# Optimization experiments

Hardware: AMD Instinct MI355X
Metric: run time of the kernel (lower is better)

## Reference

```python
import jax, jax.numpy as jnp
import numpy as np

N_NODES = 50000
N_EDGES = 800000
NODE_FEAT = 3
HID = 64
L = 4


def setup_inputs() -> dict:
    key = jax.random.key(0)
    ks = jax.random.split(key, 16)
    s = 0.05  # init scale
    inp = {
        'node_pos': jax.random.normal(ks[0], (N_NODES, 3), jnp.float32),
        'node_features': jax.random.normal(ks[1], (N_NODES, NODE_FEAT), jnp.float32),
        'edge_index': jax.random.randint(ks[2], (2, N_EDGES), 0, N_NODES, jnp.int64),
        # encoders
        'enc_w': jax.random.normal(ks[3], (NODE_FEAT, HID), jnp.float32) * s,
        'enc_b': jnp.zeros((HID,), jnp.float32),
        'edge_enc_w': jax.random.normal(ks[4], (3, HID), jnp.float32) * s,
        'edge_enc_b': jnp.zeros((HID,), jnp.float32),
        # stacked per-layer GNOLayer params
        'ew1': jax.random.normal(ks[5], (L, 3 * HID, HID), jnp.float32) * s,
        'eb1': jnp.zeros((L, HID), jnp.float32),
        'ew2': jax.random.normal(ks[6], (L, HID, HID), jnp.float32) * s,
        'eb2': jnp.zeros((L, HID), jnp.float32),
        'nw1': jax.random.normal(ks[7], (L, 2 * HID, HID), jnp.float32) * s,
        'nb1': jnp.zeros((L, HID), jnp.float32),
        'nw2': jax.random.normal(ks[8], (L, HID, HID), jnp.float32) * s,
        'nb2': jnp.zeros((L, HID), jnp.float32),
        # decoder
        'dec_w': jax.random.normal(ks[9], (HID, 1), jnp.float32) * s,
        'dec_b': jnp.zeros((1,), jnp.float32),
    }
    return inp


def reference(node_pos, node_features, edge_index, enc_w, enc_b, edge_enc_w,
              edge_enc_b, ew1, eb1, ew2, eb2, nw1, nb1, nw2, nb2, dec_w, dec_b):
    src, dst = edge_index[0], edge_index[1]
    edge_vec = node_pos[dst] - node_pos[src]            # [E, 3]
    h = node_features @ enc_w + enc_b                   # [N, H]
    e = edge_vec @ edge_enc_w + edge_enc_b              # [E, H]

    def layer(h, p):
        w1, b1, w2, b2, m1, c1, m2, c2 = p
        edge_in = jnp.concatenate([h[src], h[dst], e], axis=-1)   # [E, 3H]
        msg = jax.nn.relu(edge_in @ w1 + b1) @ w2 + b2            # [E, H]
        agg = jax.ops.segment_sum(msg, dst, num_segments=N_NODES)  # [N, H]
        node_in = jnp.concatenate([h, agg], axis=-1)              # [N, 2H]
        return jax.nn.relu(node_in @ m1 + c1) @ m2 + c2, None

    h, _ = jax.lax.scan(layer, h, (ew1, eb1, ew2, eb2, nw1, nb1, nw2, nb2))
    return h @ dec_w + dec_b                            # [N, 1]
```

## Files before the change

### kernel.cpp

```cpp
#include <hip/hip_runtime.h>

#define N_NODES 50000
#define N_EDGES 800000
#define HID 64
#define LAYERS 4
#define EP_NPB 32
#define EP_CAP 2048

typedef unsigned short u16;
typedef __attribute__((ext_vector_type(8))) __bf16 bf16x8;
typedef __attribute__((ext_vector_type(8))) unsigned short u16x8;
typedef __attribute__((ext_vector_type(4))) float f32x4;
typedef _Float16 h2 __attribute__((ext_vector_type(2)));

__device__ __forceinline__ u16 f2bf(float f) {
  unsigned u = __builtin_bit_cast(unsigned, f);
  u += 0x7fffu + ((u >> 16) & 1u);
  return (u16)(u >> 16);
}
__device__ __forceinline__ float bf2f(u16 s) {
  return __builtin_bit_cast(float, ((unsigned)s) << 16);
}
__device__ __forceinline__ u16 f2h(float f) {
  return __builtin_bit_cast(u16, (_Float16)f);
}
__device__ __forceinline__ unsigned pkadd(unsigned a, unsigned b) {
  h2 r = __builtin_bit_cast(h2, a) + __builtin_bit_cast(h2, b);
  return __builtin_bit_cast(unsigned, r);
}
__device__ __forceinline__ unsigned pkmax0(unsigned x) {
  unsigned r, z = 0u;
  asm("v_pk_max_f16 %0, %1, %2" : "=v"(r) : "v"(x), "v"(z));
  return r;
}

__global__ __launch_bounds__(256) void init_kernel(
    const float* __restrict__ nf, const float* __restrict__ enc_w,
    const float* __restrict__ enc_b,
    const float* __restrict__ ew1, const float* __restrict__ eb1,
    const float* __restrict__ ew2, const float* __restrict__ eb2,
    const float* __restrict__ nw1, const float* __restrict__ nw2,
    const float* __restrict__ edge_enc_w, const float* __restrict__ edge_enc_b,
    u16* __restrict__ h, u16* W1abT, float* Wvx, float* b1x,
    u16* NB1T, float* bb2, u16* M2T, int* __restrict__ cnt) {
  const int T = gridDim.x * 256;
  int tid = blockIdx.x * 256 + threadIdx.x;
  for (int i = tid; i < N_NODES; i += T) cnt[i] = 0;
  {
    const int szA = LAYERS * 128 * 64, szV = LAYERS * 3 * 64, szB = LAYERS * 64;
    const int szN = LAYERS * 64 * 128, szb2 = LAYERS * 64, szM = LAYERS * 64 * 64;
    const int tot = szA + szV + szB + szN + szb2 + szM;
    for (int i = tid; i < tot; i += T) {
      int idx = i;
      if (idx < szA) {
        int l = idx / (128 * 64); int r = idx % (128 * 64);
        int nfc = r / 64; int k = r % 64;
        int half = nfc >> 6, f = nfc & 63;
        W1abT[idx] = f2bf(ew1[(l * 192 + half * 64 + k) * 64 + f]);
        continue;
      }
      idx -= szA;
      if (idx < szV) {
        int l = idx / 192, r = idx % 192, a = r / 64, f = r % 64;
        float s = 0.f;
        for (int m = 0; m < 64; ++m) s += edge_enc_w[a * 64 + m] * ew1[(l * 192 + 128 + m) * 64 + f];
        Wvx[idx] = s;
        continue;
      }
      idx -= szV;
      if (idx < szB) {
        int l = idx / 64, f = idx % 64;
        float s = eb1[l * 64 + f];
        for (int m = 0; m < 64; ++m) s += edge_enc_b[m] * ew1[(l * 192 + 128 + m) * 64 + f];
        b1x[idx] = s;
        continue;
      }
      idx -= szB;
      if (idx < szN) {
        int l = idx / 8192, r = idx % 8192, f = r / 128, k = r % 128;
        float v;
        if (k < 64) v = nw1[(l * 128 + k) * 64 + f];
        else {
          int j = k - 64; float s = 0.f;
          for (int g = 0; g < 64; ++g)
            s += ew2[(l * 64 + j) * 64 + g] * nw1[(l * 128 + 64 + g) * 64 + f];
          v = s;
        }
        NB1T[idx] = f2bf(v);
        continue;
      }
      idx -= szN;
      if (idx < szb2) {
        int l = idx / 64, f = idx % 64;
        float s = 0.f;
        for (int g = 0; g < 64; ++g) s += eb2[l * 64 + g] * nw1[(l * 128 + 64 + g) * 64 + f];
        bb2[idx] = s;
        continue;
      }
      idx -= szb2;
      int l = idx / 4096, r = idx % 4096, f = r / 64, k = r % 64;
      M2T[idx] = f2bf(nw2[(l * 64 + k) * 64 + f]);
    }
  }
  for (int i = tid; i < N_NODES * 8; i += T) {
    int n = i >> 3, j0 = (i & 7) * 8;
    float x0 = nf[n * 3 + 0], x1 = nf[n * 3 + 1], x2 = nf[n * 3 + 2];
    u16x8 v;
#pragma unroll
    for (int j = 0; j < 8; ++j) {
      int jj = j0 + j;
      float s = enc_b[jj] + x0 * enc_w[jj] + x1 * enc_w[64 + jj] + x2 * enc_w[128 + jj];
      v[j] = f2bf(s);
    }
    *(u16x8*)(h + (size_t)n * 64 + j0) = v;
  }
}

__global__ __launch_bounds__(256) void hist_kernel(const int* __restrict__ dstA,
                                                   int* __restrict__ cnt,
                                                   int* __restrict__ rank) {
  int idx = blockIdx.x * 256 + threadIdx.x;
  if (idx < N_EDGES) rank[idx] = atomicAdd(&cnt[dstA[idx]], 1);
}

#define SCAN_NBLK 25
__global__ __launch_bounds__(256) void scan1_kernel(const int* __restrict__ cnt,
                                                    int* __restrict__ offs,
                                                    int* __restrict__ partials) {
  __shared__ int sm[2048];
  __shared__ int ws2[256];
  int t = threadIdx.x, b = blockIdx.x;
  int base = b * 2048;
#pragma unroll
  for (int i = 0; i < 8; ++i) {
    int idx = base + i * 256 + t;
    sm[i * 256 + t] = (idx < N_NODES) ? cnt[idx] : 0;
  }
  __syncthreads();
  int loc[8]; int s = 0;
#pragma unroll
  for (int i = 0; i < 8; ++i) { loc[i] = s; s += sm[t * 8 + i]; }
  ws2[t] = s;
  __syncthreads();
  for (int off = 1; off < 256; off <<= 1) {
    int u = (t >= off) ? ws2[t - off] : 0;
    __syncthreads();
    ws2[t] += u;
    __syncthreads();
  }
  int tbase = (t > 0) ? ws2[t - 1] : 0;
  if (t == 255) partials[b] = ws2[255];
#pragma unroll
  for (int i = 0; i < 8; ++i) {
    int idx = base + t * 8 + i;
    if (idx < N_NODES) offs[idx] = tbase + loc[i];
  }
}

__global__ __launch_bounds__(256) void scan3_kernel(int* __restrict__ offs,
                                                    const int* __restrict__ partials) {
  __shared__ int pref;
  int blk = (blockIdx.x * 256) >> 11;
  if (threadIdx.x == 0) {
    int s = 0;
    for (int i = 0; i < blk; ++i) s += partials[i];
    pref = s;
  }
  __syncthreads();
  int idx = blockIdx.x * 256 + threadIdx.x;
  if (idx < N_NODES) offs[idx] += pref;
}

__global__ __launch_bounds__(256) void scatter_kernel(const int* __restrict__ ei,
                                                      const int* __restrict__ offs,
                                                      const int* __restrict__ rank,
                                                      int* __restrict__ srcB) {
  int idx = blockIdx.x * 256 + threadIdx.x;
  if (idx >= N_EDGES) return;
  int s = ei[idx], d = ei[N_EDGES + idx];
  srcB[offs[d] + rank[idx]] = s << 7;
}

__global__ __launch_bounds__(256) void su_kernel(const u16* __restrict__ h,
                                                 const u16* __restrict__ W1abT,
                                                 const float* __restrict__ Wvx,
                                                 const float* __restrict__ b1x,
                                                 const float* __restrict__ pos,
                                                 u16* __restrict__ Sarr,
                                                 u16* __restrict__ Uarr, int layer) {
  __shared__ float sPos[192];
  int t = threadIdx.x;
  int lane = t & 63, wvi = t >> 6;
  int n16 = lane & 15, quad = lane >> 4;
  int n0 = blockIdx.x * 64;
  if (t < 192) {
    int idx = n0 * 3 + t;
    sPos[t] = (idx < N_NODES * 3) ? pos[idx] : 0.f;
  }
  __syncthreads();

  bf16x8 B[2][2];
  float w0[2], w1[2], w2[2], bb[2]; bool isU[2];
#pragma unroll
  for (int nt = 0; nt < 2; ++nt) {
    int col = wvi * 32 + nt * 16 + n16;
    const u16* p = W1abT + (size_t)(layer * 128 + col) * 64 + quad * 8;
    B[nt][0] = __builtin_bit_cast(bf16x8, *(const u16x8*)(p));
    B[nt][1] = __builtin_bit_cast(bf16x8, *(const u16x8*)(p + 32));
    int f = col & 63; isU[nt] = col >= 64;
    w0[nt] = Wvx[(layer * 3 + 0) * 64 + f];
    w1[nt] = Wvx[(layer * 3 + 1) * 64 + f];
    w2[nt] = Wvx[(layer * 3 + 2) * 64 + f];
    bb[nt] = b1x[layer * 64 + f];
  }
  f32x4 acc[4][2];
#pragma unroll
  for (int m = 0; m < 4; ++m)
#pragma unroll
    for (int nt = 0; nt < 2; ++nt) acc[m][nt] = (f32x4){0.f, 0.f, 0.f, 0.f};

#pragma unroll
  for (int m = 0; m < 4; ++m) {
    int row = n0 + m * 16 + n16;
    if (row >= N_NODES) row = N_NODES - 1;
    const u16* hp = h + (size_t)row * 64 + quad * 8;
    bf16x8 a0 = __builtin_bit_cast(bf16x8, *(const u16x8*)(hp));
    bf16x8 a1 = __builtin_bit_cast(bf16x8, *(const u16x8*)(hp + 32));
#pragma unroll
    for (int nt = 0; nt < 2; ++nt) {
      acc[m][nt] = __builtin_amdgcn_mfma_f32_16x16x32_bf16(a0, B[nt][0], acc[m][nt], 0, 0, 0);
      acc[m][nt] = __builtin_amdgcn_mfma_f32_16x16x32_bf16(a1, B[nt][1], acc[m][nt], 0, 0, 0);
    }
  }
#pragma unroll
  for (int m = 0; m < 4; ++m)
#pragma unroll
    for (int nt = 0; nt < 2; ++nt) {
      int col = wvi * 32 + nt * 16 + n16;
      int f = col & 63;
#pragma unroll
      for (int r = 0; r < 4; ++r) {
        int e = m * 16 + quad * 4 + r;
        int grow = n0 + e;
        if (grow < N_NODES) {
          float P = sPos[e * 3] * w0[nt] + sPos[e * 3 + 1] * w1[nt] + sPos[e * 3 + 2] * w2[nt];
          if (!isU[nt]) Sarr[(size_t)grow * 64 + f] = f2h(acc[m][nt][r] - P);
          else          Uarr[(size_t)grow * 64 + f] = f2h(acc[m][nt][r] + P + bb[nt]);
        }
      }
    }
}

__global__ __launch_bounds__(256) void ep_kernel(const u16* __restrict__ Sarr,
                                                 const u16* __restrict__ Uarr,
                                                 const int* __restrict__ srcB,
                                                 const int* __restrict__ offs,
                                                 u16* __restrict__ aggH) {
  __shared__ int sIdx[EP_CAP];
  __shared__ int sOff[EP_NPB + 1];
  int t = threadIdx.x;
  int lane = t & 63, wvi = t >> 6;
  int c = lane & 31, half = lane >> 5;
  unsigned cbu = (unsigned)(c << 2);
  int d0b = blockIdx.x * EP_NPB;
  if (t <= EP_NPB) {
    int d = d0b + t;
    sOff[t] = (d < N_NODES) ? offs[d] : N_EDGES;
  }
  __syncthreads();
  int eS = sOff[0];
  int nE = sOff[EP_NPB] - eS;
  bool fit = (nE <= EP_CAP);
  if (fit) {
    for (int i = t; i < nE; i += 256) sIdx[i] = srcB[eS + i];
    if (t == 0 && nE < EP_CAP) sIdx[nE] = 0;
  }
  __syncthreads();

  const char* __restrict__ Sb = (const char*)Sarr;
  const char* __restrict__ Ub = (const char*)Uarr;
  for (int i = 0; i < 8; i += 2) {
    int lnA = wvi * 8 + i, lnB = lnA + 1;
    int dA = d0b + lnA, dB = d0b + lnB;
    int e0A = sOff[lnA], degA = sOff[lnA + 1] - e0A;
    int e0B = sOff[lnB], degB = sOff[lnB + 1] - e0B;
    int dAc = dA < N_NODES ? dA : N_NODES - 1;
    int dBc = dB < N_NODES ? dB : N_NODES - 1;
    unsigned upA = *(const unsigned*)(Ub + (size_t)dAc * 128 + cbu);
    unsigned upB = *(const unsigned*)(Ub + (size_t)dBc * 128 + cbu);
    float saA = 0.f, sbA = 0.f, saB = 0.f, sbB = 0.f;
    int relA = (degA > 0) ? (e0A - eS) : 0;
    int relB = (degB > 0) ? (e0B - eS) : 0;
    int g0A = (degA > 0) ? e0A : 0;
    int g0B = (degB > 0) ? e0B : 0;
    int degMin = degA < degB ? degA : degB;
    int degMax = degA > degB ? degA : degB;
    int fullr = degMin >> 4;
    int rmax = (degMax + 15) >> 4;
    if (fit) {
      int r = 0;
      for (; r < fullr; ++r) {
        int base = r * 16 + half;
        unsigned wA[8], wB[8];
#pragma unroll
        for (int k = 0; k < 8; ++k) {
          int j = base + 2 * k;
          unsigned oA = (unsigned)sIdx[relA + j] + cbu;
          wA[k] = *(const unsigned*)(Sb + oA);
          unsigned oB = (unsigned)sIdx[relB + j] + cbu;
          wB[k] = *(const unsigned*)(Sb + oB);
        }
        unsigned pA = 0u, pB = 0u;
#pragma unroll
        for (int k = 0; k < 8; ++k) {
          pA = pkadd(pA, pkmax0(pkadd(wA[k], upA)));
          pB = pkadd(pB, pkmax0(pkadd(wB[k], upB)));
        }
        h2 hA2 = __builtin_bit_cast(h2, pA);
        h2 hB2 = __builtin_bit_cast(h2, pB);
        saA += (float)hA2[0]; sbA += (float)hA2[1];
        saB += (float)hB2[0]; sbB += (float)hB2[1];
      }
      for (; r < rmax; ++r) {
        int base = r * 16 + half;
        unsigned wA[8], wB[8]; bool okA[8], okB[8];
#pragma unroll
        for (int k = 0; k < 8; ++k) {
          int j = base + 2 * k;
          okA[k] = j < degA;
          unsigned oA = (unsigned)sIdx[relA + (okA[k] ? j : 0)] + cbu;
          wA[k] = *(const unsigned*)(Sb + oA);
          okB[k] = j < degB;
          unsigned oB = (unsigned)sIdx[relB + (okB[k] ? j : 0)] + cbu;
          wB[k] = *(const unsigned*)(Sb + oB);
        }
        unsigned pA = 0u, pB = 0u;
#pragma unroll
        for (int k = 0; k < 8; ++k) {
          unsigned zA = pkmax0(pkadd(wA[k], upA));
          pA = pkadd(pA, okA[k] ? zA : 0u);
          unsigned zB = pkmax0(pkadd(wB[k], upB));
          pB = pkadd(pB, okB[k] ? zB : 0u);
        }
        h2 hA2 = __builtin_bit_cast(h2, pA);
        h2 hB2 = __builtin_bit_cast(h2, pB);
        saA += (float)hA2[0]; sbA += (float)hA2[1];
        saB += (float)hB2[0]; sbB += (float)hB2[1];
      }
    } else {
      for (int r = 0; r < rmax; ++r) {
        int base = r * 16 + half;
        unsigned wA[8], wB[8]; bool okA[8], okB[8];
#pragma unroll
        for (int k = 0; k < 8; ++k) {
          int j = base + 2 * k;
          okA[k] = j < degA;
          unsigned oA = (unsigned)srcB[g0A + (okA[k] ? j : 0)] + cbu;
          wA[k] = *(const unsigned*)(Sb + oA);
          okB[k] = j < degB;
          unsigned oB = (unsigned)srcB[g0B + (okB[k] ? j : 0)] + cbu;
          wB[k] = *(const unsigned*)(Sb + oB);
        }
        unsigned pA = 0u, pB = 0u;
#pragma unroll
        for (int k = 0; k < 8; ++k) {
          unsigned zA = pkmax0(pkadd(wA[k], upA));
          pA = pkadd(pA, okA[k] ? zA : 0u);
          unsigned zB = pkmax0(pkadd(wB[k], upB));
          pB = pkadd(pB, okB[k] ? zB : 0u);
        }
        h2 hA2 = __builtin_bit_cast(h2, pA);
        h2 hB2 = __builtin_bit_cast(h2, pB);
        saA += (float)hA2[0]; sbA += (float)hA2[1];
        saB += (float)hB2[0]; sbB += (float)hB2[1];
      }
    }
    saA += __shfl_xor(saA, 32);  sbA += __shfl_xor(sbA, 32);
    saB += __shfl_xor(saB, 32);  sbB += __shfl_xor(sbB, 32);
    if (half == 0) {
      if (dA < N_NODES) {
        unsigned pk = (unsigned)f2bf(saA) | ((unsigned)f2bf(sbA) << 16);
        *(unsigned*)((char*)aggH + (size_t)dA * 128 + cbu) = pk;
      }
      if (dB < N_NODES) {
        unsigned pk = (unsigned)f2bf(saB) | ((unsigned)f2bf(sbB) << 16);
        *(unsigned*)((char*)aggH + (size_t)dB * 128 + cbu) = pk;
      }
    }
  }
}

__global__ __launch_bounds__(256) void node_kernel(
    const u16* __restrict__ h, const u16* __restrict__ aggH,
    const int* __restrict__ cnt,
    const u16* __restrict__ NB1T, const float* __restrict__ nb1,
    const float* __restrict__ bb2,
    const u16* __restrict__ M2T, const float* __restrict__ nb2,
    u16* __restrict__ h2, int layer,
    const u16* __restrict__ W1abT, const float* __restrict__ Wvx,
    const float* __restrict__ b1x, const float* __restrict__ pos,
    u16* __restrict__ Sarr, u16* __restrict__ Uarr,
    const float* __restrict__ dec_w, const float* __restrict__ dec_b,
    float* __restrict__ out) {
  __shared__ u16 Hs[64 * 72];
  __shared__ float sDeg[64];
  __shared__ float sPos[192];
  __shared__ float sRed[64][4];
  int t = threadIdx.x;
  int lane = t & 63, wvi = t >> 6;
  int n16 = lane & 15, quad = lane >> 4;
  int F = wvi * 16;
  int n0 = blockIdx.x * 64;

  if (t < 64) {
    int gn = n0 + t;
    sDeg[t] = (gn < N_NODES) ? (float)cnt[gn] : 0.f;
  }
  if (t >= 64 && t < 256) {
    int i = t - 64;
    int idx = n0 * 3 + i;
    sPos[i] = (idx < N_NODES * 3) ? pos[idx] : 0.f;
  }

  bf16x8 B1[4], B2[2];
  {
    const u16* p = NB1T + (size_t)(layer * 64 + F + n16) * 128 + quad * 8;
#pragma unroll
    for (int ks = 0; ks < 4; ++ks) B1[ks] = __builtin_bit_cast(bf16x8, *(const u16x8*)(p + ks * 32));
    const u16* q = M2T + (size_t)(layer * 64 + F + n16) * 64 + quad * 8;
#pragma unroll
    for (int ks = 0; ks < 2; ++ks) B2[ks] = __builtin_bit_cast(bf16x8, *(const u16x8*)(q + ks * 32));
  }
  float bias1 = nb1[layer * 64 + F + n16];
  float bb2f = bb2[layer * 64 + F + n16];
  float bias2 = nb2[layer * 64 + F + n16];
  __syncthreads();

  f32x4 acc[4];
#pragma unroll
  for (int m = 0; m < 4; ++m) acc[m] = (f32x4){0.f, 0.f, 0.f, 0.f};
#pragma unroll
  for (int m = 0; m < 4; ++m) {
    int row = n0 + m * 16 + n16;
    if (row >= N_NODES) row = N_NODES - 1;
    const u16* hp = h + (size_t)row * 64 + quad * 8;
    const u16* ap = aggH + (size_t)row * 64 + quad * 8;
    bf16x8 a0 = __builtin_bit_cast(bf16x8, *(const u16x8*)(hp));
    bf16x8 a1 = __builtin_bit_cast(bf16x8, *(const u16x8*)(hp + 32));
    bf16x8 a2 = __builtin_bit_cast(bf16x8, *(const u16x8*)(ap));
    bf16x8 a3 = __builtin_bit_cast(bf16x8, *(const u16x8*)(ap + 32));
    acc[m] = __builtin_amdgcn_mfma_f32_16x16x32_bf16(a0, B1[0], acc[m], 0, 0, 0);
    acc[m] = __builtin_amdgcn_mfma_f32_16x16x32_bf16(a1, B1[1], acc[m], 0, 0, 0);
    acc[m] = __builtin_amdgcn_mfma_f32_16x16x32_bf16(a2, B1[2], acc[m], 0, 0, 0);
    acc[m] = __builtin_amdgcn_mfma_f32_16x16x32_bf16(a3, B1[3], acc[m], 0, 0, 0);
  }
#pragma unroll
  for (int m = 0; m < 4; ++m)
#pragma unroll
    for (int r = 0; r < 4; ++r) {
      int e = m * 16 + quad * 4 + r;
      float v = acc[m][r] + bias1 + sDeg[e] * bb2f;
      v = v > 0.f ? v : 0.f;
      Hs[e * 72 + F + n16] = f2bf(v);
    }
  __syncthreads();

  float c2[4][4];
#pragma unroll
  for (int m = 0; m < 4; ++m) {
    const u16* hp = Hs + (m * 16 + n16) * 72 + quad * 8;
    f32x4 c = (f32x4){0.f, 0.f, 0.f, 0.f};
#pragma unroll
    for (int ks = 0; ks < 2; ++ks) {
      bf16x8 a = __builtin_bit_cast(bf16x8, *(const u16x8*)(hp + ks * 32));
      c = __builtin_amdgcn_mfma_f32_16x16x32_bf16(a, B2[ks], c, 0, 0, 0);
    }
#pragma unroll
    for (int r = 0; r < 4; ++r) c2[m][r] = c[r] + bias2;
  }
  __syncthreads();

#pragma unroll
  for (int m = 0; m < 4; ++m)
#pragma unroll
    for (int r = 0; r < 4; ++r) {
      int e = m * 16 + quad * 4 + r;
      u16 hv = f2bf(c2[m][r]);
      Hs[e * 72 + F + n16] = hv;
      int gn = n0 + e;
      if (layer < LAYERS - 1 && gn < N_NODES)
        h2[(size_t)gn * 64 + F + n16] = hv;
    }
  __syncthreads();

  if (layer < LAYERS - 1) {
    int lp = layer + 1;
    bf16x8 B3[2][2];
    float w0[2], w1[2], w2[2], bb[2]; bool isU[2];
#pragma unroll
    for (int nt = 0; nt < 2; ++nt) {
      int col = wvi * 32 + nt * 16 + n16;
      const u16* p = W1abT + (size_t)(lp * 128 + col) * 64 + quad * 8;
      B3[nt][0] = __builtin_bit_cast(bf16x8, *(const u16x8*)(p));
      B3[nt][1] = __builtin_bit_cast(bf16x8, *(const u16x8*)(p + 32));
      int f = col & 63; isU[nt] = col >= 64;
      w0[nt] = Wvx[(lp * 3 + 0) * 64 + f];
      w1[nt] = Wvx[(lp * 3 + 1) * 64 + f];
      w2[nt] = Wvx[(lp * 3 + 2) * 64 + f];
      bb[nt] = b1x[lp * 64 + f];
    }
    f32x4 a3[4][2];
#pragma unroll
    for (int m = 0; m < 4; ++m)
#pragma unroll
      for (int nt = 0; nt < 2; ++nt) a3[m][nt] = (f32x4){0.f, 0.f, 0.f, 0.f};
#pragma unroll
    for (int m = 0; m < 4; ++m) {
      const u16* hp = Hs + (m * 16 + n16) * 72 + quad * 8;
      bf16x8 a0 = __builtin_bit_cast(bf16x8, *(const u16x8*)(hp));
      bf16x8 a1 = __builtin_bit_cast(bf16x8, *(const u16x8*)(hp + 32));
#pragma unroll
      for (int nt = 0; nt < 2; ++nt) {
        a3[m][nt] = __builtin_amdgcn_mfma_f32_16x16x32_bf16(a0, B3[nt][0], a3[m][nt], 0, 0, 0);
        a3[m][nt] = __builtin_amdgcn_mfma_f32_16x16x32_bf16(a1, B3[nt][1], a3[m][nt], 0, 0, 0);
      }
    }
#pragma unroll
    for (int m = 0; m < 4; ++m)
#pragma unroll
      for (int nt = 0; nt < 2; ++nt) {
        int col = wvi * 32 + nt * 16 + n16;
        int f = col & 63;
#pragma unroll
        for (int r = 0; r < 4; ++r) {
          int e = m * 16 + quad * 4 + r;
          int grow = n0 + e;
          if (grow < N_NODES) {
            float P = sPos[e * 3] * w0[nt] + sPos[e * 3 + 1] * w1[nt] + sPos[e * 3 + 2] * w2[nt];
            if (!isU[nt]) Sarr[(size_t)grow * 64 + f] = f2h(a3[m][nt][r] - P);
            else          Uarr[(size_t)grow * 64 + f] = f2h(a3[m][nt][r] + P + bb[nt]);
          }
        }
      }
  } else {
    int e = t >> 2, part = t & 3;
    float s = 0.f;
#pragma unroll
    for (int j = 0; j < 16; ++j)
      s += bf2f(Hs[e * 72 + part * 16 + j]) * dec_w[part * 16 + j];
    sRed[e][part] = s;
    __syncthreads();
    if (part == 0) {
      int gn = n0 + e;
      if (gn < N_NODES)
        out[gn] = sRed[e][0] + sRed[e][1] + sRed[e][2] + sRed[e][3] + dec_b[0];
    }
  }
}

extern "C" void kernel_launch(void* const* d_in, const int* in_sizes, int n_in,
                              void* d_out, int out_size, void* d_ws, size_t ws_size,
                              hipStream_t stream) {
  const float* node_pos   = (const float*)d_in[0];
  const float* node_feat  = (const float*)d_in[1];
  const int*   edge_index = (const int*)d_in[2];
  const float* enc_w      = (const float*)d_in[3];
  const float* enc_b      = (const float*)d_in[4];
  const float* edge_enc_w = (const float*)d_in[5];
  const float* edge_enc_b = (const float*)d_in[6];
  const float* ew1        = (const float*)d_in[7];
  const float* eb1        = (const float*)d_in[8];
  const float* ew2        = (const float*)d_in[9];
  const float* eb2        = (const float*)d_in[10];
  const float* nw1        = (const float*)d_in[11];
  const float* nb1        = (const float*)d_in[12];
  const float* nw2        = (const float*)d_in[13];
  const float* nb2        = (const float*)d_in[14];
  const float* dec_w      = (const float*)d_in[15];
  const float* dec_b      = (const float*)d_in[16];
  float* out = (float*)d_out;

  char* ws = (char*)d_ws;
  size_t off = 0;
  u16*    hA    = (u16*)(ws + off);    off += (size_t)N_NODES * 64 * 2;
  u16*    hB    = (u16*)(ws + off);    off += (size_t)N_NODES * 64 * 2;
  u16*    Sarr  = (u16*)(ws + off);    off += (size_t)N_NODES * 64 * 2;
  u16*    Uarr  = (u16*)(ws + off);    off += (size_t)N_NODES * 64 * 2;
  u16*    aggH  = (u16*)(ws + off);    off += (size_t)N_NODES * 64 * 2;
  u16*    W1abT = (u16*)(ws + off);    off += (size_t)LAYERS * 128 * 64 * 2;
  float*  Wvx   = (float*)(ws + off);  off += (size_t)LAYERS * 3 * 64 * 4;
  float*  b1x   = (float*)(ws + off);  off += (size_t)LAYERS * 64 * 4;
  u16*    NB1T  = (u16*)(ws + off);    off += (size_t)LAYERS * 64 * 128 * 2;
  float*  bb2   = (float*)(ws + off);  off += (size_t)LAYERS * 64 * 4;
  u16*    M2T   = (u16*)(ws + off);    off += (size_t)LAYERS * 64 * 64 * 2;
  int*    cnt      = (int*)(ws + off); off += (size_t)N_NODES * 4;
  int*    offsB    = (int*)(ws + off); off += (size_t)N_NODES * 4;
  int*    partials = (int*)(ws + off); off += 32 * 4;
  int*    rank     = (int*)(ws + off); off += (size_t)N_EDGES * 4;
  int*    srcB     = (int*)(ws + off); off += (size_t)N_EDGES * 4;

  const int* dstA = edge_index + N_EDGES;
  const int NBLK = (N_NODES + 63) / 64;
  const int EP_GRID = (N_NODES + EP_NPB - 1) / EP_NPB;

  init_kernel<<<1024, 256, 0, stream>>>(
      node_feat, enc_w, enc_b, ew1, eb1, ew2, eb2, nw1, nw2,
      edge_enc_w, edge_enc_b, hA, W1abT, Wvx, b1x, NB1T, bb2, M2T, cnt);

  hist_kernel<<<(N_EDGES + 255) / 256, 256, 0, stream>>>(dstA, cnt, rank);
  scan1_kernel<<<SCAN_NBLK, 256, 0, stream>>>(cnt, offsB, partials);
  scan3_kernel<<<(N_NODES + 255) / 256, 256, 0, stream>>>(offsB, partials);
  scatter_kernel<<<(N_EDGES + 255) / 256, 256, 0, stream>>>(edge_index, offsB, rank, srcB);

  su_kernel<<<NBLK, 256, 0, stream>>>(hA, W1abT, Wvx, b1x, node_pos, Sarr, Uarr, 0);

  u16* hcur = hA; u16* hnext = hB;
  for (int l = 0; l < LAYERS; ++l) {
    ep_kernel<<<EP_GRID, 256, 0, stream>>>(Sarr, Uarr, srcB, offsB, aggH);
    node_kernel<<<NBLK, 256, 0, stream>>>(hcur, aggH, cnt, NB1T, nb1, bb2, M2T, nb2,
                                          hnext, l, W1abT, Wvx, b1x, node_pos,
                                          Sarr, Uarr, dec_w, dec_b, out);
    u16* tmp = hcur; hcur = hnext; hnext = tmp;
  }
}
```

Before: 342.2 us.

## Fuse edge aggregation and node update into one per-layer kernel

Merges the per-layer edge-aggregation kernel and the node MLP kernel into one layer_kernel working on 32 nodes per block. The aggregate stays in shared memory instead of round-tripping through global memory. S/U buffers are now double-buffered so the fused kernel can read this layer's S/U while writing the next layer's. The node encoder also moves into the first S/U kernel, which uses a shared-memory tile of h. This saves a launch and a global write and read per layer, at the cost of a larger shared-memory footprint and half-size MFMA tiles in the node phase.

```diff
diff --git a/kernel.cpp b/kernel.cpp
--- a/kernel.cpp
+++ b/kernel.cpp
@@ -4,14 +4,14 @@
 #define N_EDGES 800000
 #define HID 64
 #define LAYERS 4
-#define EP_NPB 32
 #define EP_CAP 2048
+#define SCAN_NBLK 25
 
 typedef unsigned short u16;
 typedef __attribute__((ext_vector_type(8))) __bf16 bf16x8;
 typedef __attribute__((ext_vector_type(8))) unsigned short u16x8;
 typedef __attribute__((ext_vector_type(4))) float f32x4;
-typedef _Float16 h2 __attribute__((ext_vector_type(2)));
+typedef _Float16 f16x2 __attribute__((ext_vector_type(2)));
 
 __device__ __forceinline__ u16 f2bf(float f) {
   unsigned u = __builtin_bit_cast(unsigned, f);
@@ -25,7 +25,7 @@
   return __builtin_bit_cast(u16, (_Float16)f);
 }
 __device__ __forceinline__ unsigned pkadd(unsigned a, unsigned b) {
-  h2 r = __builtin_bit_cast(h2, a) + __builtin_bit_cast(h2, b);
+  f16x2 r = __builtin_bit_cast(f16x2, a) + __builtin_bit_cast(f16x2, b);
   return __builtin_bit_cast(unsigned, r);
 }
 __device__ __forceinline__ unsigned pkmax0(unsigned x) {
@@ -35,84 +35,68 @@
 }
 
 __global__ __launch_bounds__(256) void init_kernel(
-    const float* __restrict__ nf, const float* __restrict__ enc_w,
-    const float* __restrict__ enc_b,
     const float* __restrict__ ew1, const float* __restrict__ eb1,
     const float* __restrict__ ew2, const float* __restrict__ eb2,
     const float* __restrict__ nw1, const float* __restrict__ nw2,
     const float* __restrict__ edge_enc_w, const float* __restrict__ edge_enc_b,
-    u16* __restrict__ h, u16* W1abT, float* Wvx, float* b1x,
+    u16* W1abT, float* Wvx, float* b1x,
     u16* NB1T, float* bb2, u16* M2T, int* __restrict__ cnt) {
   const int T = gridDim.x * 256;
   int tid = blockIdx.x * 256 + threadIdx.x;
   for (int i = tid; i < N_NODES; i += T) cnt[i] = 0;
-  {
-    const int szA = LAYERS * 128 * 64, szV = LAYERS * 3 * 64, szB = LAYERS * 64;
-    const int szN = LAYERS * 64 * 128, szb2 = LAYERS * 64, szM = LAYERS * 64 * 64;
-    const int tot = szA + szV + szB + szN + szb2 + szM;
-    for (int i = tid; i < tot; i += T) {
-      int idx = i;
-      if (idx < szA) {
-        int l = idx / (128 * 64); int r = idx % (128 * 64);
-        int nfc = r / 64; int k = r % 64;
-        int half = nfc >> 6, f = nfc & 63;
-        W1abT[idx] = f2bf(ew1[(l * 192 + half * 64 + k) * 64 + f]);
-        continue;
+  const int szA = LAYERS * 128 * 64, szV = LAYERS * 3 * 64, szB = LAYERS * 64;
+  const int szN = LAYERS * 64 * 128, szb2 = LAYERS * 64, szM = LAYERS * 64 * 64;
+  const int tot = szA + szV + szB + szN + szb2 + szM;
+  for (int i = tid; i < tot; i += T) {
+    int idx = i;
+    if (idx < szA) {
+      int l = idx / (128 * 64); int r = idx % (128 * 64);
+      int nfc = r / 64; int k = r % 64;
+      int half = nfc >> 6, f = nfc & 63;
+      W1abT[idx] = f2bf(ew1[(l * 192 + half * 64 + k) * 64 + f]);
+      continue;
+    }
+    idx -= szA;
+    if (idx < szV) {
+      int l = idx / 192, r = idx % 192, a = r / 64, f = r % 64;
+      float s = 0.f;
+      for (int m = 0; m < 64; ++m) s += edge_enc_w[a * 64 + m] * ew1[(l * 192 + 128 + m) * 64 + f];
+      Wvx[idx] = s;
+      continue;
+    }
+    idx -= szV;
+    if (idx < szB) {
+      int l = idx / 64, f = idx % 64;
+      float s = eb1[l * 64 + f];
+      for (int m = 0; m < 64; ++m) s += edge_enc_b[m] * ew1[(l * 192 + 128 + m) * 64 + f];
+      b1x[idx] = s;
+      continue;
+    }
+    idx -= szB;
+    if (idx < szN) {
+      int l = idx / 8192, r = idx % 8192, f = r / 128, k = r % 128;
+      float v;
+      if (k < 64) v = nw1[(l * 128 + k) * 64 + f];
+      else {
+        int j = k - 64; float s = 0.f;
+        for (int g = 0; g < 64; ++g)
+          s += ew2[(l * 64 + j) * 64 + g] * nw1[(l * 128 + 64 + g) * 64 + f];
+        v = s;
       }
-      idx -= szA;
-      if (idx < szV) {
-        int l = idx / 192, r = idx % 192, a = r / 64, f = r % 64;
-        float s = 0.f;
-        for (int m = 0; m < 64; ++m) s += edge_enc_w[a * 64 + m] * ew1[(l * 192 + 128 + m) * 64 + f];
-        Wvx[idx] = s;
-        continue;
-      }
-      idx -= szV;
-      if (idx < szB) {
-        int l = idx / 64, f = idx % 64;
-        float s = eb1[l * 64 + f];
-        for (int m = 0; m < 64; ++m) s += edge_enc_b[m] * ew1[(l * 192 + 128 + m) * 64 + f];
-        b1x[idx] = s;
-        continue;
-      }
-      idx -= szB;
-      if (idx < szN) {
-        int l = idx / 8192, r = idx % 8192, f = r / 128, k = r % 128;
-        float v;
-        if (k < 64) v = nw1[(l * 128 + k) * 64 + f];
-        else {
-          int j = k - 64; float s = 0.f;
-          for (int g = 0; g < 64; ++g)
-            s += ew2[(l * 64 + j) * 64 + g] * nw1[(l * 128 + 64 + g) * 64 + f];
-          v = s;
-        }
-        NB1T[idx] = f2bf(v);
-        continue;
-      }
-      idx -= szN;
-      if (idx < szb2) {
-        int l = idx / 64, f = idx % 64;
-        float s = 0.f;
-        for (int g = 0; g < 64; ++g) s += eb2[l * 64 + g] * nw1[(l * 128 + 64 + g) * 64 + f];
-        bb2[idx] = s;
-        continue;
-      }
-      idx -= szb2;
-      int l = idx / 4096, r = idx % 4096, f = r / 64, k = r % 64;
-      M2T[idx] = f2bf(nw2[(l * 64 + k) * 64 + f]);
-    }
-  }
-  for (int i = tid; i < N_NODES * 8; i += T) {
-    int n = i >> 3, j0 = (i & 7) * 8;
-    float x0 = nf[n * 3 + 0], x1 = nf[n * 3 + 1], x2 = nf[n * 3 + 2];
-    u16x8 v;
-#pragma unroll
-    for (int j = 0; j < 8; ++j) {
-      int jj = j0 + j;
-      float s = enc_b[jj] + x0 * enc_w[jj] + x1 * enc_w[64 + jj] + x2 * enc_w[128 + jj];
-      v[j] = f2bf(s);
-    }
-    *(u16x8*)(h + (size_t)n * 64 + j0) = v;
+      NB1T[idx] = f2bf(v);
+      continue;
+    }
+    idx -= szN;
+    if (idx < szb2) {
+      int l = idx / 64, f = idx % 64;
+      float s = 0.f;
+      for (int g = 0; g < 64; ++g) s += eb2[l * 64 + g] * nw1[(l * 128 + 64 + g) * 64 + f];
+      bb2[idx] = s;
+      continue;
+    }
+    idx -= szb2;
+    int l = idx / 4096, r = idx % 4096, f = r / 64, k = r % 64;
+    M2T[idx] = f2bf(nw2[(l * 64 + k) * 64 + f]);
   }
 }
 
@@ -123,7 +107,6 @@
   if (idx < N_EDGES) rank[idx] = atomicAdd(&cnt[dstA[idx]], 1);
 }
 
-#define SCAN_NBLK 25
 __global__ __launch_bounds__(256) void scan1_kernel(const int* __restrict__ cnt,
                                                     int* __restrict__ offs,
                                                     int* __restrict__ partials) {
@@ -181,21 +164,44 @@
   srcB[offs[d] + rank[idx]] = s << 7;
 }
 
-__global__ __launch_bounds__(256) void su_kernel(const u16* __restrict__ h,
-                                                 const u16* __restrict__ W1abT,
-                                                 const float* __restrict__ Wvx,
-                                                 const float* __restrict__ b1x,
-                                                 const float* __restrict__ pos,
-                                                 u16* __restrict__ Sarr,
-                                                 u16* __restrict__ Uarr, int layer) {
+__global__ __launch_bounds__(256) void encsu_kernel(
+    const float* __restrict__ nf, const float* __restrict__ enc_w,
+    const float* __restrict__ enc_b,
+    const u16* __restrict__ W1abT, const float* __restrict__ Wvx,
+    const float* __restrict__ b1x, const float* __restrict__ pos,
+    u16* __restrict__ h, u16* __restrict__ Sarr, u16* __restrict__ Uarr) {
+  __shared__ u16 hT[64 * 72];
   __shared__ float sPos[192];
+  __shared__ float sNf[192];
   int t = threadIdx.x;
   int lane = t & 63, wvi = t >> 6;
   int n16 = lane & 15, quad = lane >> 4;
   int n0 = blockIdx.x * 64;
   if (t < 192) {
     int idx = n0 * 3 + t;
-    sPos[t] = (idx < N_NODES * 3) ? pos[idx] : 0.f;
+    bool ok = idx < N_NODES * 3;
+    sPos[t] = ok ? pos[idx] : 0.f;
+    sNf[t] = ok ? nf[idx] : 0.f;
+  }
+  __syncthreads();
+  {
+    int n = t >> 2, g = t & 3;
+    float x0 = sNf[n * 3], x1 = sNf[n * 3 + 1], x2 = sNf[n * 3 + 2];
+    u16x8 v0, v1;
+#pragma unroll
+    for (int j = 0; j < 8; ++j) {
+      int jj = g * 16 + j;
+      v0[j] = f2bf(enc_b[jj] + x0 * enc_w[jj] + x1 * enc_w[64 + jj] + x2 * enc_w[128 + jj]);
+      int jj2 = jj + 8;
+      v1[j] = f2bf(enc_b[jj2] + x0 * enc_w[jj2] + x1 * enc_w[64 + jj2] + x2 * enc_w[128 + jj2]);
+    }
+    *(u16x8*)(hT + n * 72 + g * 16) = v0;
+    *(u16x8*)(hT + n * 72 + g * 16 + 8) = v1;
+    int gn = n0 + n;
+    if (gn < N_NODES) {
+      *(u16x8*)(h + (size_t)gn * 64 + g * 16) = v0;
+      *(u16x8*)(h + (size_t)gn * 64 + g * 16 + 8) = v1;
+    }
   }
   __syncthreads();
 
@@ -204,26 +210,23 @@
 #pragma unroll
   for (int nt = 0; nt < 2; ++nt) {
     int col = wvi * 32 + nt * 16 + n16;
-    const u16* p = W1abT + (size_t)(layer * 128 + col) * 64 + quad * 8;
+    const u16* p = W1abT + (size_t)col * 64 + quad * 8;
     B[nt][0] = __builtin_bit_cast(bf16x8, *(const u16x8*)(p));
     B[nt][1] = __builtin_bit_cast(bf16x8, *(const u16x8*)(p + 32));
     int f = col & 63; isU[nt] = col >= 64;
-    w0[nt] = Wvx[(layer * 3 + 0) * 64 + f];
-    w1[nt] = Wvx[(layer * 3 + 1) * 64 + f];
-    w2[nt] = Wvx[(layer * 3 + 2) * 64 + f];
-    bb[nt] = b1x[layer * 64 + f];
+    w0[nt] = Wvx[f];
+    w1[nt] = Wvx[64 + f];
+    w2[nt] = Wvx[128 + f];
+    bb[nt] = b1x[f];
   }
   f32x4 acc[4][2];
 #pragma unroll
   for (int m = 0; m < 4; ++m)
 #pragma unroll
     for (int nt = 0; nt < 2; ++nt) acc[m][nt] = (f32x4){0.f, 0.f, 0.f, 0.f};
-
 #pragma unroll
   for (int m = 0; m < 4; ++m) {
-    int row = n0 + m * 16 + n16;
-    if (row >= N_NODES) row = N_NODES - 1;
-    const u16* hp = h + (size_t)row * 64 + quad * 8;
+    const u16* hp = hT + (m * 16 + n16) * 72 + quad * 8;
     bf16x8 a0 = __builtin_bit_cast(bf16x8, *(const u16x8*)(hp));
     bf16x8 a1 = __builtin_bit_cast(bf16x8, *(const u16x8*)(hp + 32));
 #pragma unroll
@@ -251,25 +254,43 @@
     }
 }
 
-__global__ __launch_bounds__(256) void ep_kernel(const u16* __restrict__ Sarr,
-                                                 const u16* __restrict__ Uarr,
-                                                 const int* __restrict__ srcB,
-                                                 const int* __restrict__ offs,
-                                                 u16* __restrict__ aggH) {
+__global__ __launch_bounds__(256) void layer_kernel(
+    const u16* __restrict__ h, const int* __restrict__ srcB,
+    const int* __restrict__ offs,
+    const u16* __restrict__ Sr, const u16* __restrict__ Ur,
+    const u16* __restrict__ NB1T, const float* __restrict__ nb1,
+    const float* __restrict__ bb2,
+    const u16* __restrict__ M2T, const float* __restrict__ nb2,
+    u16* __restrict__ hnext, int layer,
+    const u16* __restrict__ W1abT, const float* __restrict__ Wvx,
+    const float* __restrict__ b1x, const float* __restrict__ pos,
+    u16* __restrict__ Sw, u16* __restrict__ Uw,
+    const float* __restrict__ dec_w, const float* __restrict__ dec_b,
+    float* __restrict__ out) {
   __shared__ int sIdx[EP_CAP];
-  __shared__ int sOff[EP_NPB + 1];
+  __shared__ int sOff[33];
+  __shared__ u16 aggT[32 * 72];
+  __shared__ u16 Hs[32 * 72];
+  __shared__ float sPos[96];
+  __shared__ float sRed[32][8];
   int t = threadIdx.x;
   int lane = t & 63, wvi = t >> 6;
-  int c = lane & 31, half = lane >> 5;
-  unsigned cbu = (unsigned)(c << 2);
-  int d0b = blockIdx.x * EP_NPB;
-  if (t <= EP_NPB) {
-    int d = d0b + t;
+  int n16 = lane & 15, quad = lane >> 4;
+  int F = wvi * 16;
+  int n0 = blockIdx.x * 32;
+
+  if (t <= 32) {
+    int d = n0 + t;
     sOff[t] = (d < N_NODES) ? offs[d] : N_EDGES;
   }
+  if (t >= 64 && t < 160) {
+    int i = t - 64;
+    int idx = n0 * 3 + i;
+    sPos[i] = (idx < N_NODES * 3) ? pos[idx] : 0.f;
+  }
   __syncthreads();
   int eS = sOff[0];
-  int nE = sOff[EP_NPB] - eS;
+  int nE = sOff[32] - eS;
   bool fit = (nE <= EP_CAP);
   if (fit) {
     for (int i = t; i < nE; i += 256) sIdx[i] = srcB[eS + i];
@@ -277,150 +298,112 @@
   }
   __syncthreads();
 
-  const char* __restrict__ Sb = (const char*)Sarr;
-  const char* __restrict__ Ub = (const char*)Uarr;
-  for (int i = 0; i < 8; i += 2) {
-    int lnA = wvi * 8 + i, lnB = lnA + 1;
-    int dA = d0b + lnA, dB = d0b + lnB;
-    int e0A = sOff[lnA], degA = sOff[lnA + 1] - e0A;
-    int e0B = sOff[lnB], degB = sOff[lnB + 1] - e0B;
-    int dAc = dA < N_NODES ? dA : N_NODES - 1;
-    int dBc = dB < N_NODES ? dB : N_NODES - 1;
-    unsigned upA = *(const unsigned*)(Ub + (size_t)dAc * 128 + cbu);
-    unsigned upB = *(const unsigned*)(Ub + (size_t)dBc * 128 + cbu);
-    float saA = 0.f, sbA = 0.f, saB = 0.f, sbB = 0.f;
-    int relA = (degA > 0) ? (e0A - eS) : 0;
-    int relB = (degB > 0) ? (e0B - eS) : 0;
-    int g0A = (degA > 0) ? e0A : 0;
-    int g0B = (degB > 0) ? e0B : 0;
-    int degMin = degA < degB ? degA : degB;
-    int degMax = degA > degB ? degA : degB;
-    int fullr = degMin >> 4;
-    int rmax = (degMax + 15) >> 4;
-    if (fit) {
-      int r = 0;
-      for (; r < fullr; ++r) {
-        int base = r * 16 + half;
-        unsigned wA[8], wB[8];
-#pragma unroll
-        for (int k = 0; k < 8; ++k) {
-          int j = base + 2 * k;
-          unsigned oA = (unsigned)sIdx[relA + j] + cbu;
-          wA[k] = *(const unsigned*)(Sb + oA);
-          unsigned oB = (unsigned)sIdx[relB + j] + cbu;
-          wB[k] = *(const unsigned*)(Sb + oB);
+  {
+    int c = lane & 31, half = lane >> 5;
+    unsigned cbu = (unsigned)(c << 2);
+    const char* __restrict__ Sb = (const char*)Sr;
+    const char* __restrict__ Ub = (const char*)Ur;
+    for (int i = 0; i < 8; i += 2) {
+      int lnA = wvi * 8 + i;
+      int dA = n0 + lnA;
+      int e0A = sOff[lnA], degA = sOff[lnA + 1] - e0A;
+      int e0B = sOff[lnA + 1], degB = sOff[lnA + 2] - e0B;
+      int dAc = dA < N_NODES ? dA : N_NODES - 1;
+      int dBc = (dA + 1) < N_NODES ? (dA + 1) : N_NODES - 1;
+      unsigned upA = *(const unsigned*)(Ub + (size_t)dAc * 128 + cbu);
+      unsigned upB = *(const unsigned*)(Ub + (size_t)dBc * 128 + cbu);
+      float saA = 0.f, sbA = 0.f, saB = 0.f, sbB = 0.f;
+      int relA = (degA > 0) ? (e0A - eS) : 0;
+      int relB = (degB > 0) ? (e0B - eS) : 0;
+      int g0A = (degA > 0) ? e0A : 0;
+      int g0B = (degB > 0) ? e0B : 0;
+      int degMin = degA < degB ? degA : degB;
+      int degMax = degA > degB ? degA : degB;
+      int fullr = degMin >> 4;
+      int rmax = (degMax + 15) >> 4;
+      if (fit) {
+        int r = 0;
+        for (; r < fullr; ++r) {
+          int base = r * 16 + half;
+          unsigned wA[8], wB[8];
+#pragma unroll
+          for (int kk = 0; kk < 8; ++kk) {
+            int j = base + 2 * kk;
+            wA[kk] = *(const unsigned*)(Sb + (unsigned)sIdx[relA + j] + cbu);
+            wB[kk] = *(const unsigned*)(Sb + (unsigned)sIdx[relB + j] + cbu);
+          }
+          unsigned pA = 0u, pB = 0u;
+#pragma unroll
+          for (int kk = 0; kk < 8; ++kk) {
+            pA = pkadd(pA, pkmax0(pkadd(wA[kk], upA)));
+            pB = pkadd(pB, pkmax0(pkadd(wB[kk], upB)));
+          }
+          f16x2 hA2 = __builtin_bit_cast(f16x2, pA);
+          f16x2 hB2 = __builtin_bit_cast(f16x2, pB);
+          saA += (float)hA2[0]; sbA += (float)hA2[1];
+          saB += (float)hB2[0]; sbB += (float)hB2[1];
         }
-        unsigned pA = 0u, pB = 0u;
-#pragma unroll
-        for (int k = 0; k < 8; ++k) {
-          pA = pkadd(pA, pkmax0(pkadd(wA[k], upA)));
-          pB = pkadd(pB, pkmax0(pkadd(wB[k], upB)));
+        for (; r < rmax; ++r) {
+          int base = r * 16 + half;
+          unsigned wA[8], wB[8]; bool okA[8], okB[8];
+#pragma unroll
+          for (int kk = 0; kk < 8; ++kk) {
+            int j = base + 2 * kk;
+            okA[kk] = j < degA;
+            wA[kk] = *(const unsigned*)(Sb + (unsigned)sIdx[relA + (okA[kk] ? j : 0)] + cbu);
+            okB[kk] = j < degB;
+            wB[kk] = *(const unsigned*)(Sb + (unsigned)sIdx[relB + (okB[kk] ? j : 0)] + cbu);
+          }
+          unsigned pA = 0u, pB = 0u;
+#pragma unroll
+          for (int kk = 0; kk < 8; ++kk) {
+            unsigned zA = pkmax0(pkadd(wA[kk], upA));
+            pA = pkadd(pA, okA[kk] ? zA : 0u);
+            unsigned zB = pkmax0(pkadd(wB[kk], upB));
+            pB = pkadd(pB, okB[kk] ? zB : 0u);
+          }
+          f16x2 hA2 = __builtin_bit_cast(f16x2, pA);
+          f16x2 hB2 = __builtin_bit_cast(f16x2, pB);
+          saA += (float)hA2[0]; sbA += (float)hA2[1];
+          saB += (float)hB2[0]; sbB += (float)hB2[1];
         }
-        h2 hA2 = __builtin_bit_cast(h2, pA);
-        h2 hB2 = __builtin_bit_cast(h2, pB);
-        saA += (float)hA2[0]; sbA += (float)hA2[1];
-        saB += (float)hB2[0]; sbB += (float)hB2[1];
+      } else {
+        for (int r = 0; r < rmax; ++r) {
+          int base = r * 16 + half;
+          unsigned wA[8], wB[8]; bool okA[8], okB[8];
+#pragma unroll
+          for (int kk = 0; kk < 8; ++kk) {
+            int j = base + 2 * kk;
+            okA[kk] = j < degA;
+            wA[kk] = *(const unsigned*)(Sb + (unsigned)srcB[g0A + (okA[kk] ? j : 0)] + cbu);
+            okB[kk] = j < degB;
+            wB[kk] = *(const unsigned*)(Sb + (unsigned)srcB[g0B + (okB[kk] ? j : 0)] + cbu);
+          }
+          unsigned pA = 0u, pB = 0u;
+#pragma unroll
+          for (int kk = 0; kk < 8; ++kk) {
+            unsigned zA = pkmax0(pkadd(wA[kk], upA));
+            pA = pkadd(pA, okA[kk] ? zA : 0u);
+            unsigned zB = pkmax0(pkadd(wB[kk], upB));
+            pB = pkadd(pB, okB[kk] ? zB : 0u);
+          }
+          f16x2 hA2 = __builtin_bit_cast(f16x2, pA);
+          f16x2 hB2 = __builtin_bit_cast(f16x2, pB);
+          saA += (float)hA2[0]; sbA += (float)hA2[1];
+          saB += (float)hB2[0]; sbB += (float)hB2[1];
+        }
       }
-      for (; r < rmax; ++r) {
-        int base = r * 16 + half;
-        unsigned wA[8], wB[8]; bool okA[8], okB[8];
-#pragma unroll
-        for (int k = 0; k < 8; ++k) {
-          int j = base + 2 * k;
-          okA[k] = j < degA;
-          unsigned oA = (unsigned)sIdx[relA + (okA[k] ? j : 0)] + cbu;
-          wA[k] = *(const unsigned*)(Sb + oA);
-          okB[k] = j < degB;
-          unsigned oB = (unsigned)sIdx[relB + (okB[k] ? j : 0)] + cbu;
-          wB[k] = *(const unsigned*)(Sb + oB);
-        }
-        unsigned pA = 0u, pB = 0u;
-#pragma unroll
-        for (int k = 0; k < 8; ++k) {
-          unsigned zA = pkmax0(pkadd(wA[k], upA));
-          pA = pkadd(pA, okA[k] ? zA : 0u);
-          unsigned zB = pkmax0(pkadd(wB[k], upB));
-          pB = pkadd(pB, okB[k] ? zB : 0u);
-        }
-        h2 hA2 = __builtin_bit_cast(h2, pA);
-        h2 hB2 = __builtin_bit_cast(h2, pB);
-        saA += (float)hA2[0]; sbA += (float)hA2[1];
-        saB += (float)hB2[0]; sbB += (float)hB2[1];
+      saA += __shfl_xor(saA, 32);  sbA += __shfl_xor(sbA, 32);
+      saB += __shfl_xor(saB, 32);  sbB += __shfl_xor(sbB, 32);
+      if (half == 0) {
+        unsigned pk = (unsigned)f2bf(saA) | ((unsigned)f2bf(sbA) << 16);
+        *(unsigned*)((char*)aggT + (size_t)lnA * 144 + cbu) = pk;
+        unsigned pk2 = (unsigned)f2bf(saB) | ((unsigned)f2bf(sbB) << 16);
+        *(unsigned*)((char*)aggT + (size_t)(lnA + 1) * 144 + cbu) = pk2;
       }
-    } else {
-      for (int r = 0; r < rmax; ++r) {
-        int base = r * 16 + half;
-        unsigned wA[8], wB[8]; bool okA[8], okB[8];
-#pragma unroll
-        for (int k = 0; k < 8; ++k) {
-          int j = base + 2 * k;
-          okA[k] = j < degA;
-          unsigned oA = (unsigned)srcB[g0A + (okA[k] ? j : 0)] + cbu;
-          wA[k] = *(const unsigned*)(Sb + oA);
-          okB[k] = j < degB;
-          unsigned oB = (unsigned)srcB[g0B + (okB[k] ? j : 0)] + cbu;
-          wB[k] = *(const unsigned*)(Sb + oB);
-        }
-        unsigned pA = 0u, pB = 0u;
-#pragma unroll
-        for (int k = 0; k < 8; ++k) {
-          unsigned zA = pkmax0(pkadd(wA[k], upA));
-          pA = pkadd(pA, okA[k] ? zA : 0u);
-          unsigned zB = pkmax0(pkadd(wB[k], upB));
-          pB = pkadd(pB, okB[k] ? zB : 0u);
-        }
-        h2 hA2 = __builtin_bit_cast(h2, pA);
-        h2 hB2 = __builtin_bit_cast(h2, pB);
-        saA += (float)hA2[0]; sbA += (float)hA2[1];
-        saB += (float)hB2[0]; sbB += (float)hB2[1];
-      }
-    }
-    saA += __shfl_xor(saA, 32);  sbA += __shfl_xor(sbA, 32);
-    saB += __shfl_xor(saB, 32);  sbB += __shfl_xor(sbB, 32);
-    if (half == 0) {
-      if (dA < N_NODES) {
-        unsigned pk = (unsigned)f2bf(saA) | ((unsigned)f2bf(sbA) << 16);
-        *(unsigned*)((char*)aggH + (size_t)dA * 128 + cbu) = pk;
-      }
-      if (dB < N_NODES) {
-        unsigned pk = (unsigned)f2bf(saB) | ((unsigned)f2bf(sbB) << 16);
-        *(unsigned*)((char*)aggH + (size_t)dB * 128 + cbu) = pk;
-      }
-    }
-  }
-}
-
-__global__ __launch_bounds__(256) void node_kernel(
-    const u16* __restrict__ h, const u16* __restrict__ aggH,
-    const int* __restrict__ cnt,
-    const u16* __restrict__ NB1T, const float* __restrict__ nb1,
-    const float* __restrict__ bb2,
-    const u16* __restrict__ M2T, const float* __restrict__ nb2,
-    u16* __restrict__ h2, int layer,
-    const u16* __restrict__ W1abT, const float* __restrict__ Wvx,
-    const float* __restrict__ b1x, const float* __restrict__ pos,
-    u16* __restrict__ Sarr, u16* __restrict__ Uarr,
-    const float* __restrict__ dec_w, const float* __restrict__ dec_b,
-    float* __restrict__ out) {
-  __shared__ u16 Hs[64 * 72];
-  __shared__ float sDeg[64];
-  __shared__ float sPos[192];
-  __shared__ float sRed[64][4];
-  int t = threadIdx.x;
-  int lane = t & 63, wvi = t >> 6;
-  int n16 = lane & 15, quad = lane >> 4;
-  int F = wvi * 16;
-  int n0 = blockIdx.x * 64;
-
-  if (t < 64) {
-    int gn = n0 + t;
-    sDeg[t] = (gn < N_NODES) ? (float)cnt[gn] : 0.f;
-  }
-  if (t >= 64 && t < 256) {
-    int i = t - 64;
-    int idx = n0 * 3 + i;
-    sPos[i] = (idx < N_NODES * 3) ? pos[idx] : 0.f;
-  }
+    }
+  }
+  __syncthreads();
 
   bf16x8 B1[4], B2[2];
   {
@@ -434,17 +417,16 @@
   float bias1 = nb1[layer * 64 + F + n16];
   float bb2f = bb2[layer * 64 + F + n16];
   float bias2 = nb2[layer * 64 + F + n16];
-  __syncthreads();
-
-  f32x4 acc[4];
-#pragma unroll
-  for (int m = 0; m < 4; ++m) acc[m] = (f32x4){0.f, 0.f, 0.f, 0.f};
-#pragma unroll
-  for (int m = 0; m < 4; ++m) {
+
+  f32x4 acc[2];
+#pragma unroll
+  for (int m = 0; m < 2; ++m) acc[m] = (f32x4){0.f, 0.f, 0.f, 0.f};
+#pragma unroll
+  for (int m = 0; m < 2; ++m) {
     int row = n0 + m * 16 + n16;
     if (row >= N_NODES) row = N_NODES - 1;
     const u16* hp = h + (size_t)row * 64 + quad * 8;
-    const u16* ap = aggH + (size_t)row * 64 + quad * 8;
+    const u16* ap = aggT + (m * 16 + n16) * 72 + quad * 8;
     bf16x8 a0 = __builtin_bit_cast(bf16x8, *(const u16x8*)(hp));
     bf16x8 a1 = __builtin_bit_cast(bf16x8, *(const u16x8*)(hp + 32));
     bf16x8 a2 = __builtin_bit_cast(bf16x8, *(const u16x8*)(ap));
@@ -455,33 +437,34 @@
     acc[m] = __builtin_amdgcn_mfma_f32_16x16x32_bf16(a3, B1[3], acc[m], 0, 0, 0);
   }
 #pragma unroll
-  for (int m = 0; m < 4; ++m)
+  for (int m = 0; m < 2; ++m)
 #pragma unroll
     for (int r = 0; r < 4; ++r) {
       int e = m * 16 + quad * 4 + r;
-      float v = acc[m][r] + bias1 + sDeg[e] * bb2f;
+      float dg = (float)(sOff[e + 1] - sOff[e]);
+      float v = acc[m][r] + bias1 + dg * bb2f;
       v = v > 0.f ? v : 0.f;
       Hs[e * 72 + F + n16] = f2bf(v);
     }
   __syncthreads();
 
-  float c2[4][4];
-#pragma unroll
-  for (int m = 0; m < 4; ++m) {
+  float c2[2][4];
+#pragma unroll
+  for (int m = 0; m < 2; ++m) {
     const u16* hp = Hs + (m * 16 + n16) * 72 + quad * 8;
-    f32x4 c = (f32x4){0.f, 0.f, 0.f, 0.f};
+    f32x4 cc = (f32x4){0.f, 0.f, 0.f, 0.f};
 #pragma unroll
     for (int ks = 0; ks < 2; ++ks) {
       bf16x8 a = __builtin_bit_cast(bf16x8, *(const u16x8*)(hp + ks * 32));
-      c = __builtin_amdgcn_mfma_f32_16x16x32_bf16(a, B2[ks], c, 0, 0, 0);
-    }
-#pragma unroll
-    for (int r = 0; r < 4; ++r) c2[m][r] = c[r] + bias2;
-  }
-  __syncthreads();
-
-#pragma unroll
-  for (int m = 0; m < 4; ++m)
+      cc = __builtin_amdgcn_mfma_f32_16x16x32_bf16(a, B2[ks], cc, 0, 0, 0);
+    }
+#pragma unroll
+    for (int r = 0; r < 4; ++r) c2[m][r] = cc[r] + bias2;
+  }
+  __syncthreads();
+
+#pragma unroll
+  for (int m = 0; m < 2; ++m)
 #pragma unroll
     for (int r = 0; r < 4; ++r) {
       int e = m * 16 + quad * 4 + r;
@@ -489,7 +472,7 @@
       Hs[e * 72 + F + n16] = hv;
       int gn = n0 + e;
       if (layer < LAYERS - 1 && gn < N_NODES)
-        h2[(size_t)gn * 64 + F + n16] = hv;
+        hnext[(size_t)gn * 64 + F + n16] = hv;
     }
   __syncthreads();
 
@@ -509,13 +492,13 @@
       w2[nt] = Wvx[(lp * 3 + 2) * 64 + f];
       bb[nt] = b1x[lp * 64 + f];
     }
-    f32x4 a3[4][2];
-#pragma unroll
-    for (int m = 0; m < 4; ++m)
+    f32x4 a3[2][2];
+#pragma unroll
+    for (int m = 0; m < 2; ++m)
 #pragma unroll
       for (int nt = 0; nt < 2; ++nt) a3[m][nt] = (f32x4){0.f, 0.f, 0.f, 0.f};
 #pragma unroll
-    for (int m = 0; m < 4; ++m) {
+    for (int m = 0; m < 2; ++m) {
       const u16* hp = Hs + (m * 16 + n16) * 72 + quad * 8;
       bf16x8 a0 = __builtin_bit_cast(bf16x8, *(const u16x8*)(hp));
       bf16x8 a1 = __builtin_bit_cast(bf16x8, *(const u16x8*)(hp + 32));
@@ -526,7 +509,7 @@
       }
     }
 #pragma unroll
-    for (int m = 0; m < 4; ++m)
+    for (int m = 0; m < 2; ++m)
 #pragma unroll
       for (int nt = 0; nt < 2; ++nt) {
         int col = wvi * 32 + nt * 16 + n16;
@@ -537,23 +520,27 @@
           int grow = n0 + e;
           if (grow < N_NODES) {
             float P = sPos[e * 3] * w0[nt] + sPos[e * 3 + 1] * w1[nt] + sPos[e * 3 + 2] * w2[nt];
-            if (!isU[nt]) Sarr[(size_t)grow * 64 + f] = f2h(a3[m][nt][r] - P);
-            else          Uarr[(size_t)grow * 64 + f] = f2h(a3[m][nt][r] + P + bb[nt]);
+            if (!isU[nt]) Sw[(size_t)grow * 64 + f] = f2h(a3[m][nt][r] - P);
+            else          Uw[(size_t)grow * 64 + f] = f2h(a3[m][nt][r] + P + bb[nt]);
           }
         }
       }
   } else {
-    int e = t >> 2, part = t & 3;
+    int e = t >> 3, part = t & 7;
     float s = 0.f;
 #pragma unroll
-    for (int j = 0; j < 16; ++j)
-      s += bf2f(Hs[e * 72 + part * 16 + j]) * dec_w[part * 16 + j];
+    for (int j = 0; j < 8; ++j)
+      s += bf2f(Hs[e * 72 + part * 8 + j]) * dec_w[part * 8 + j];
     sRed[e][part] = s;
     __syncthreads();
     if (part == 0) {
       int gn = n0 + e;
-      if (gn < N_NODES)
-        out[gn] = sRed[e][0] + sRed[e][1] + sRed[e][2] + sRed[e][3] + dec_b[0];
+      if (gn < N_NODES) {
+        float acc8 = dec_b[0];
+#pragma unroll
+        for (int p2 = 0; p2 < 8; ++p2) acc8 += sRed[e][p2];
+        out[gn] = acc8;
+      }
     }
   }
 }
@@ -584,9 +571,10 @@
   size_t off = 0;
   u16*    hA    = (u16*)(ws + off);    off += (size_t)N_NODES * 64 * 2;
   u16*    hB    = (u16*)(ws + off);    off += (size_t)N_NODES * 64 * 2;
-  u16*    Sarr  = (u16*)(ws + off);    off += (size_t)N_NODES * 64 * 2;
-  u16*    Uarr  = (u16*)(ws + off);    off += (size_t)N_NODES * 64 * 2;
-  u16*    aggH  = (u16*)(ws + off);    off += (size_t)N_NODES * 64 * 2;
+  u16*    S0    = (u16*)(ws + off);    off += (size_t)N_NODES * 64 * 2;
+  u16*    U0    = (u16*)(ws + off);    off += (size_t)N_NODES * 64 * 2;
+  u16*    S1    = (u16*)(ws + off);    off += (size_t)N_NODES * 64 * 2;
+  u16*    U1    = (u16*)(ws + off);    off += (size_t)N_NODES * 64 * 2;
   u16*    W1abT = (u16*)(ws + off);    off += (size_t)LAYERS * 128 * 64 * 2;
   float*  Wvx   = (float*)(ws + off);  off += (size_t)LAYERS * 3 * 64 * 4;
   float*  b1x   = (float*)(ws + off);  off += (size_t)LAYERS * 64 * 4;
@@ -600,26 +588,30 @@
   int*    srcB     = (int*)(ws + off); off += (size_t)N_EDGES * 4;
 
   const int* dstA = edge_index + N_EDGES;
-  const int NBLK = (N_NODES + 63) / 64;
-  const int EP_GRID = (N_NODES + EP_NPB - 1) / EP_NPB;
-
-  init_kernel<<<1024, 256, 0, stream>>>(
-      node_feat, enc_w, enc_b, ew1, eb1, ew2, eb2, nw1, nw2,
-      edge_enc_w, edge_enc_b, hA, W1abT, Wvx, b1x, NB1T, bb2, M2T, cnt);
+  const int NBLK64 = (N_NODES + 63) / 64;
+  const int NBLK32 = (N_NODES + 31) / 32;
+
+  init_kernel<<<512, 256, 0, stream>>>(
+      ew1, eb1, ew2, eb2, nw1, nw2, edge_enc_w, edge_enc_b,
+      W1abT, Wvx, b1x, NB1T, bb2, M2T, cnt);
 
   hist_kernel<<<(N_EDGES + 255) / 256, 256, 0, stream>>>(dstA, cnt, rank);
   scan1_kernel<<<SCAN_NBLK, 256, 0, stream>>>(cnt, offsB, partials);
   scan3_kernel<<<(N_NODES + 255) / 256, 256, 0, stream>>>(offsB, partials);
   scatter_kernel<<<(N_EDGES + 255) / 256, 256, 0, stream>>>(edge_index, offsB, rank, srcB);
 
-  su_kernel<<<NBLK, 256, 0, stream>>>(hA, W1abT, Wvx, b1x, node_pos, Sarr, Uarr, 0);
-
-  u16* hcur = hA; u16* hnext = hB;
+  encsu_kernel<<<NBLK64, 256, 0, stream>>>(node_feat, enc_w, enc_b,
+                                           W1abT, Wvx, b1x, node_pos, hA, S0, U0);
+
+  u16 *hc = hA, *hn = hB, *Sr = S0, *Ur = U0, *Sw = S1, *Uw = U1;
   for (int l = 0; l < LAYERS; ++l) {
-    ep_kernel<<<EP_GRID, 256, 0, stream>>>(Sarr, Uarr, srcB, offsB, aggH);
-    node_kernel<<<NBLK, 256, 0, stream>>>(hcur, aggH, cnt, NB1T, nb1, bb2, M2T, nb2,
-                                          hnext, l, W1abT, Wvx, b1x, node_pos,
-                                          Sarr, Uarr, dec_w, dec_b, out);
-    u16* tmp = hcur; hcur = hnext; hnext = tmp;
-  }
-}
+    layer_kernel<<<NBLK32, 256, 0, stream>>>(hc, srcB, offsB, Sr, Ur,
+                                             NB1T, nb1, bb2, M2T, nb2,
+                                             hn, l, W1abT, Wvx, b1x, node_pos,
+                                             Sw, Uw, dec_w, dec_b, out);
+    u16* tmp;
+    tmp = hc; hc = hn; hn = tmp;
+    tmp = Sr; Sr = Sw; Sw = tmp;
+    tmp = Ur; Ur = Uw; Uw = tmp;
+  }
+}
```

Measured after the change: 312.0 us. -8.8%, faster.
